# Kernel tuning notes

Measured on AMD Instinct MI355X. Metric: run time of the kernel, lower is better.

Reference implementation:

```python
import jax, jax.numpy as jnp
import numpy as np
from jax import lax

B_, L_, D_ = 4, 2048, 256
DI, NS, DC, DTR = 512, 16, 4, 16  # d_inner=2*D, d_state, d_conv, dt_rank=ceil(D/16)
DFF = 4 * D_


def setup_inputs():
    key = jax.random.key(0)
    ks = jax.random.split(key, 20)
    rn = lambda k, s, sc=0.02: jax.random.normal(k, s, jnp.float32) * sc
    return {
        "x": jax.random.normal(ks[0], (B_, L_, D_), jnp.float32),
        "in_proj_w": rn(ks[1], (2 * DI, D_)), "in_proj_b": jnp.zeros((2 * DI,), jnp.float32),
        "conv_w": rn(ks[2], (DI, DC), 0.1), "conv_b": jnp.zeros((DI,), jnp.float32),
        "x_proj_w": rn(ks[3], (DTR + 2 * NS, DI)),
        "dt_proj_w": rn(ks[4], (DI, DTR), 0.1), "dt_proj_b": rn(ks[5], (DI,), 0.5),
        "A_log": jnp.log(jnp.tile(jnp.arange(1, NS + 1, dtype=jnp.float32), (DI, 1))),
        "D_ssm": jnp.ones((DI,), jnp.float32),
        "out_proj_w": rn(ks[6], (D_, DI)), "out_proj_b": jnp.zeros((D_,), jnp.float32),
        "ln1_g": jnp.ones((D_,), jnp.float32), "ln1_b": jnp.zeros((D_,), jnp.float32),
        "fc1_w": rn(ks[7], (DFF, D_)), "fc1_b": jnp.zeros((DFF,), jnp.float32),
        "fc2_w": rn(ks[8], (D_, DFF)), "fc2_b": jnp.zeros((D_,), jnp.float32),
        "ln2_g": jnp.ones((D_,), jnp.float32), "ln2_b": jnp.zeros((D_,), jnp.float32),
    }


def _layer_norm(x, g, b, eps=1e-5):
    m = jnp.mean(x, -1, keepdims=True)
    v = jnp.mean((x - m) ** 2, -1, keepdims=True)
    return (x - m) / jnp.sqrt(v + eps) * g + b


def _mamba(x, in_proj_w, in_proj_b, conv_w, conv_b, x_proj_w, dt_proj_w, dt_proj_b, A_log, D_ssm, out_proj_w, out_proj_b):
    B, L, D = x.shape
    xz = x @ in_proj_w.T + in_proj_b                       # [B,L,2*DI]
    xi, z = jnp.split(xz, 2, axis=-1)
    # causal depthwise conv over time
    xc = jnp.transpose(xi, (0, 2, 1))                       # [B,DI,L]
    xc = lax.conv_general_dilated(xc, conv_w[:, None, :], (1,), [(DC - 1, 0)],
                                  dimension_numbers=("NCH", "OIH", "NCH"),
                                  feature_group_count=DI)
    xi = jax.nn.silu(jnp.transpose(xc + conv_b[None, :, None], (0, 2, 1)))  # [B,L,DI]
    x_dbl = xi @ x_proj_w.T                                 # [B,L,DTR+2*NS]
    dt, Bs, Cs = jnp.split(x_dbl, [DTR, DTR + NS], axis=-1)
    dt = jax.nn.softplus(dt @ dt_proj_w.T + dt_proj_b)      # [B,L,DI]
    A = -jnp.exp(A_log)                                     # [DI,NS]
    dA = jnp.exp(dt[..., None] * A)                         # [B,L,DI,NS]
    dBu = dt[..., None] * Bs[:, :, None, :] * xi[..., None]  # [B,L,DI,NS]
    dA_t = jnp.moveaxis(dA, 1, 0)
    dBu_t = jnp.moveaxis(dBu, 1, 0)
    C_t = jnp.moveaxis(Cs, 1, 0)                            # [L,B,NS]

    def step(h, inp):
        a, bu, c = inp
        h = a * h + bu                                      # [B,DI,NS]
        y = jnp.einsum("bdn,bn->bd", h, c)
        return h, y

    h0 = jnp.zeros((B, DI, NS), x.dtype)
    _, ys = lax.scan(step, h0, (dA_t, dBu_t, C_t))
    y = jnp.moveaxis(ys, 0, 1) + xi * D_ssm                 # [B,L,DI]
    y = y * jax.nn.silu(z)
    return y @ out_proj_w.T + out_proj_b


def reference(x, in_proj_w, in_proj_b, conv_w, conv_b, x_proj_w, dt_proj_w, dt_proj_b,
              A_log, D_ssm, out_proj_w, out_proj_b, ln1_g, ln1_b, fc1_w, fc1_b,
              fc2_w, fc2_b, ln2_g, ln2_b):
    gelu = lambda t: jax.nn.gelu(t, approximate=False)
    ssm = _mamba(x, in_proj_w, in_proj_b, conv_w, conv_b, x_proj_w, dt_proj_w,
                 dt_proj_b, A_log, D_ssm, out_proj_w, out_proj_b)
    y = _layer_norm(x + ssm, ln1_g, ln1_b)                  # dropout = identity (eval)
    ffn = gelu(gelu(y @ fc1_w.T + fc1_b) @ fc2_w.T + fc2_b)
    return _layer_norm(y + ffn, ln2_g, ln2_b)
```

## Files before the change

### kernel.cpp

```cpp
#include <hip/hip_runtime.h>

typedef __bf16 bf16x8 __attribute__((ext_vector_type(8)));
typedef float  f32x4  __attribute__((ext_vector_type(4)));

#define AS1 __attribute__((address_space(1)))
#define AS3 __attribute__((address_space(3)))

__device__ __forceinline__ float bf2f(ushort u) {
    union { unsigned int i; float f; } v; v.i = ((unsigned int)u) << 16; return v.f;
}
__device__ __forceinline__ ushort f2bf(float f) {
    union { float f; unsigned int i; } v; v.f = f;
    unsigned int i = v.i;
    unsigned int r = i + 0x7FFFu + ((i >> 16) & 1u);
    return (ushort)(r >> 16);
}
__device__ __forceinline__ float bflo(unsigned int u) { return bf2f((ushort)(u & 0xFFFFu)); }
__device__ __forceinline__ float bfhi(unsigned int u) { return bf2f((ushort)(u >> 16)); }

__device__ __forceinline__ bool sniff_inline(const ushort* __restrict__ x) {
    const int lane = threadIdx.x & 63;
    int cnt = 0;
    #pragma unroll
    for (int r = 0; r < 4; r++) {
        const ushort u = x[lane + r * 64];
        const int e = (u >> 7) & 0xFF;
        if ((u & 0x7FFF) == 0 || (e >= 112 && e <= 141)) cnt++;
    }
    #pragma unroll
    for (int o = 32; o > 0; o >>= 1) cnt += __shfl_xor(cnt, o);
    return cnt >= 224;
}

struct CanonArgs {
    const void* src[20];
    int off[20];
    int total;
};

__launch_bounds__(256)
__global__ void canon_k(CanonArgs a, ushort* __restrict__ dst, ushort* __restrict__ xpw_pad,
                        const ushort* __restrict__ sniffx)
{
    const int i = blockIdx.x * 256 + threadIdx.x;
    if (i >= a.total) {
        const int j = i - a.total;
        if (j < 8192) xpw_pad[24576 + j] = 0;
        return;
    }
    const bool fl = sniff_inline(sniffx);
    int s = 0;
    #pragma unroll
    for (int t = 1; t < 20; t++) if (i >= a.off[t]) s = t;
    const int li = i - a.off[s];
    ushort v;
    if (fl) v = ((const ushort*)a.src[s])[li];
    else    v = f2bf(((const float*)a.src[s])[li]);
    dst[i] = v;
    if (s == 5) xpw_pad[li] = v;
}

template<int BM, int BN, int ACT, bool HASB, bool WF32, bool WBF16>
__launch_bounds__(256, 2)
__global__ void gemm_bt(const ushort* __restrict__ A, const ushort* __restrict__ W,
                        const ushort* __restrict__ bias,
                        float* __restrict__ Cf, ushort* __restrict__ Cb,
                        int M, int N, int K, int lda)
{
    constexpr int WMT = BM / 32;
    constexpr int WNT = BN / 32;
    __shared__ __align__(16) ushort As[BM * 32];
    __shared__ __align__(16) ushort Bs[BN * 32];
    const int tid  = threadIdx.x;
    const int wave = tid >> 6;
    const int lane = tid & 63;
    const int m0 = blockIdx.x * BM;
    const int n0 = blockIdx.y * BN;
    const int wm = (wave >> 1) * (BM / 2);
    const int wn = (wave & 1) * (BN / 2);
    const int lrow = lane & 15;
    const int quad = lane >> 4;

    f32x4 acc[WMT][WNT];
    #pragma unroll
    for (int i = 0; i < WMT; i++)
        #pragma unroll
        for (int j = 0; j < WNT; j++)
            #pragma unroll
            for (int r = 0; r < 4; r++) acc[i][j][r] = 0.f;

    for (int k0 = 0; k0 < K; k0 += 32) {
        #pragma unroll
        for (int t = 0; t < BM / 64; t++) {
            const int inst = t * 4 + wave;
            const int row  = inst * 16 + (lane >> 2);
            const int sub  = lane & 3;
            const ushort* gp = A + (size_t)(m0 + row) * lda + (k0 + sub * 8);
            __builtin_amdgcn_global_load_lds((AS1 void*)(void*)gp,
                                             (AS3 void*)(As + inst * 512), 16, 0, 0);
        }
        #pragma unroll
        for (int t = 0; t < BN / 64; t++) {
            const int inst = t * 4 + wave;
            const int row  = inst * 16 + (lane >> 2);
            const int sub  = lane & 3;
            const ushort* gp = W + (size_t)(n0 + row) * K + (k0 + sub * 8);
            __builtin_amdgcn_global_load_lds((AS1 void*)(void*)gp,
                                             (AS3 void*)(Bs + inst * 512), 16, 0, 0);
        }
        __syncthreads();
        bf16x8 afr[WMT], bfr[WNT];
        #pragma unroll
        for (int i = 0; i < WMT; i++)
            afr[i] = *(const bf16x8*)&As[(wm + i * 16 + lrow) * 32 + quad * 8];
        #pragma unroll
        for (int j = 0; j < WNT; j++)
            bfr[j] = *(const bf16x8*)&Bs[(wn + j * 16 + lrow) * 32 + quad * 8];
        #pragma unroll
        for (int i = 0; i < WMT; i++)
            #pragma unroll
            for (int j = 0; j < WNT; j++)
                acc[i][j] = __builtin_amdgcn_mfma_f32_16x16x32_bf16(afr[i], bfr[j], acc[i][j], 0, 0, 0);
        __syncthreads();
    }

    #pragma unroll
    for (int i = 0; i < WMT; i++) {
        const int gm = m0 + wm + i * 16 + quad * 4;
        #pragma unroll
        for (int j = 0; j < WNT; j++) {
            const int gn = n0 + wn + j * 16 + lrow;
            const float bv = HASB ? bf2f(bias[gn]) : 0.f;
            #pragma unroll
            for (int r = 0; r < 4; r++) {
                float v = acc[i][j][r] + bv;
                if (ACT == 1) v = 0.5f * v * (1.f + erff(v * 0.70710678118654752f));
                const size_t off = (size_t)(gm + r) * N + gn;
                if (WF32)  Cf[off] = v;
                if (WBF16) Cb[off] = f2bf(v);
            }
        }
    }
}

__launch_bounds__(256, 2)
__global__ void convxdbl_k(const ushort* __restrict__ xz, const ushort* __restrict__ cw,
                           const ushort* __restrict__ cb, const ushort* __restrict__ xpw_pad,
                           ushort* __restrict__ xc, float* __restrict__ xdbl)
{
    __shared__ __align__(16) ushort xcs[16 * 520];
    __shared__ __align__(16) ushort Bs[64 * 32];
    const int tid  = threadIdx.x;
    const int wave = tid >> 6;
    const int lane = tid & 63;
    const int T0 = blockIdx.x * 16;

    const int d8 = (tid & 63) * 8;
    const int tr = tid >> 6;
    ushort wl[32];
    *(uint4*)&wl[0]  = *(const uint4*)&cw[d8 * 4];
    *(uint4*)&wl[8]  = *(const uint4*)&cw[d8 * 4 + 8];
    *(uint4*)&wl[16] = *(const uint4*)&cw[d8 * 4 + 16];
    *(uint4*)&wl[24] = *(const uint4*)&cw[d8 * 4 + 24];
    ushort bl[8];
    *(uint4*)&bl[0] = *(const uint4*)&cb[d8];
    #pragma unroll
    for (int it = 0; it < 4; it++) {
        const int trow = it * 4 + tr;
        const int t = T0 + trow;
        const int l = t & 2047;
        float acc[8];
        #pragma unroll
        for (int j = 0; j < 8; j++) acc[j] = bf2f(bl[j]);
        #pragma unroll
        for (int k = 0; k < 4; k++) {
            const int ls = l - 3 + k;
            if (ls >= 0) {
                ushort xl[8];
                *(uint4*)&xl[0] = *(const uint4*)&xz[(size_t)(t - 3 + k) * 1024 + d8];
                #pragma unroll
                for (int j = 0; j < 8; j++) acc[j] += bf2f(xl[j]) * bf2f(wl[j * 4 + k]);
            }
        }
        ushort ol[8];
        #pragma unroll
        for (int j = 0; j < 8; j++) {
            const float s = acc[j] / (1.f + __expf(-acc[j]));
            ol[j] = f2bf(s);
        }
        *(uint4*)&xcs[trow * 520 + d8] = *(uint4*)&ol[0];
        *(uint4*)&xc[(size_t)t * 512 + d8] = *(uint4*)&ol[0];
    }
    __syncthreads();

    const int lrow = lane & 15;
    const int quad = lane >> 4;
    const int wn = wave * 16;
    f32x4 acc2 = {0.f, 0.f, 0.f, 0.f};
    for (int k0 = 0; k0 < 512; k0 += 32) {
        {
            const int row = wn + (lane >> 2);
            const int sub = lane & 3;
            const ushort* gp = xpw_pad + (size_t)row * 512 + (k0 + sub * 8);
            __builtin_amdgcn_global_load_lds((AS1 void*)(void*)gp,
                                             (AS3 void*)(Bs + wave * 512), 16, 0, 0);
        }
        __syncthreads();
        const bf16x8 afr = *(const bf16x8*)&xcs[lrow * 520 + k0 + quad * 8];
        const bf16x8 bfr = *(const bf16x8*)&Bs[wave * 512 + lrow * 32 + quad * 8];
        acc2 = __builtin_amdgcn_mfma_f32_16x16x32_bf16(afr, bfr, acc2, 0, 0, 0);
        __syncthreads();
    }
    #pragma unroll
    for (int r = 0; r < 4; r++)
        xdbl[(size_t)(T0 + quad * 4 + r) * 64 + wn + lrow] = acc2[r];
}

__launch_bounds__(256)
__global__ void scan1_k(const float* __restrict__ xdbl, const ushort* __restrict__ xc,
                        const ushort* __restrict__ dtw, const ushort* __restrict__ dtb,
                        const ushort* __restrict__ Alog, float* __restrict__ summ)
{
    __shared__ float XD[32 * 32];
    const int tid = threadIdx.x;
    const int c = blockIdx.y, b = blockIdx.z;
    const int t0 = b * 2048 + c * 32;
    for (int e = tid; e < 1024; e += 256)
        XD[e] = xdbl[(size_t)(t0 + (e >> 5)) * 64 + (e & 31)];
    __syncthreads();
    const int d = blockIdx.x * 256 + tid;

    const uint4 w0 = *(const uint4*)&dtw[d * 16];
    const uint4 w1 = *(const uint4*)&dtw[d * 16 + 8];
    const float wd[16] = { bflo(w0.x), bfhi(w0.x), bflo(w0.y), bfhi(w0.y),
                           bflo(w0.z), bfhi(w0.z), bflo(w0.w), bfhi(w0.w),
                           bflo(w1.x), bfhi(w1.x), bflo(w1.y), bfhi(w1.y),
                           bflo(w1.z), bfhi(w1.z), bflo(w1.w), bfhi(w1.w) };
    const float dtbv = bf2f(dtb[d]);

    float A[16], h[16];
    #pragma unroll
    for (int n = 0; n < 16; n++) {
        A[n] = -__expf(bf2f(Alog[d * 16 + n]));
        h[n] = 0.f;
    }
    float sdt = 0.f;
    for (int i = 0; i < 32; i++) {
        const float* Xr = &XD[i * 32];
        float s = dtbv;
        #pragma unroll
        for (int k = 0; k < 16; k++) s += Xr[k] * wd[k];
        const float dtv = (s > 15.f) ? s : __logf(1.f + __expf(s));
        const float xiv = bf2f(xc[(size_t)(t0 + i) * 512 + d]);
        const float dx = dtv * xiv;
        sdt += dtv;
        #pragma unroll
        for (int n = 0; n < 16; n++) {
            const float da = __expf(dtv * A[n]);
            h[n] = da * h[n] + dx * Xr[16 + n];
        }
    }
    const size_t base = ((size_t)(b * 64 + c) * 32) * 512 + d;
    #pragma unroll
    for (int n = 0; n < 16; n++) summ[base + (size_t)n * 512] = __expf(A[n] * sdt);
    #pragma unroll
    for (int n = 0; n < 16; n++) summ[base + (size_t)(16 + n) * 512] = h[n];
}

__launch_bounds__(512)
__global__ void combine_k(float* __restrict__ summ)
{
    const int b = blockIdx.x >> 4, n = blockIdx.x & 15;
    const int d = threadIdx.x;
    float h = 0.f;
    #pragma unroll
    for (int half = 0; half < 2; half++) {
        float p[32], hl[32], ho[32];
        #pragma unroll
        for (int c2 = 0; c2 < 32; c2++) {
            const size_t sb = ((size_t)((b * 64 + half * 32 + c2) * 32 + n)) * 512 + d;
            p[c2]  = summ[sb];
            hl[c2] = summ[sb + 8192];
        }
        #pragma unroll
        for (int c2 = 0; c2 < 32; c2++) {
            ho[c2] = h;
            h = p[c2] * h + hl[c2];
        }
        #pragma unroll
        for (int c2 = 0; c2 < 32; c2++) {
            const size_t sb = ((size_t)((b * 64 + half * 32 + c2) * 32 + n)) * 512 + d;
            summ[sb] = ho[c2];
        }
    }
}

__launch_bounds__(256)
__global__ void scan2_k(const float* __restrict__ xdbl, ushort* xc,
                        const ushort* __restrict__ dtw, const ushort* __restrict__ dtb,
                        const ushort* __restrict__ Alog, const float* __restrict__ summ,
                        const ushort* __restrict__ xz, const ushort* __restrict__ Dssm)
{
    __shared__ float XD[32 * 48];
    const int tid = threadIdx.x;
    const int c = blockIdx.y, b = blockIdx.z;
    const int t0 = b * 2048 + c * 32;
    for (int e = tid; e < 1536; e += 256)
        XD[e] = xdbl[(size_t)(t0 + (e / 48)) * 64 + (e % 48)];
    __syncthreads();
    const int d = blockIdx.x * 256 + tid;

    const uint4 w0 = *(const uint4*)&dtw[d * 16];
    const uint4 w1 = *(const uint4*)&dtw[d * 16 + 8];
    const float wd[16] = { bflo(w0.x), bfhi(w0.x), bflo(w0.y), bfhi(w0.y),
                           bflo(w0.z), bfhi(w0.z), bflo(w0.w), bfhi(w0.w),
                           bflo(w1.x), bfhi(w1.x), bflo(w1.y), bfhi(w1.y),
                           bflo(w1.z), bfhi(w1.z), bflo(w1.w), bfhi(w1.w) };
    const float dtbv = bf2f(dtb[d]);

    float A[16], h[16];
    #pragma unroll
    for (int n = 0; n < 16; n++) A[n] = -__expf(bf2f(Alog[d * 16 + n]));
    const size_t base = ((size_t)(b * 64 + c) * 32) * 512 + d;
    #pragma unroll
    for (int n = 0; n < 16; n++) h[n] = summ[base + (size_t)n * 512];
    const float Dv = bf2f(Dssm[d]);

    for (int i = 0; i < 32; i++) {
        const int t = t0 + i;
        const float* Xr = &XD[i * 48];
        float s = dtbv;
        #pragma unroll
        for (int k = 0; k < 16; k++) s += Xr[k] * wd[k];
        const float dtv = (s > 15.f) ? s : __logf(1.f + __expf(s));
        const float xiv = bf2f(xc[(size_t)t * 512 + d]);
        const float dx = dtv * xiv;
        float yv = 0.f;
        #pragma unroll
        for (int n = 0; n < 16; n++) {
            const float da = __expf(dtv * A[n]);
            h[n] = da * h[n] + dx * Xr[16 + n];
            yv += h[n] * Xr[32 + n];
        }
        yv += xiv * Dv;
        const float zv = bf2f(xz[(size_t)t * 1024 + 512 + d]);
        yv *= zv / (1.f + __expf(-zv));
        xc[(size_t)t * 512 + d] = f2bf(yv);
    }
}

template<int K, int ACT, int MODE>
__launch_bounds__(256, 2)
__global__ void gemm_ln16(const ushort* __restrict__ A, const ushort* __restrict__ W,
                          const ushort* __restrict__ bias,
                          const ushort* __restrict__ residb, const float* __restrict__ residf,
                          const ushort* __restrict__ g, const ushort* __restrict__ bvec,
                          float* __restrict__ y1f_out, ushort* __restrict__ y1b_out,
                          void* __restrict__ dout, const ushort* __restrict__ sniffx)
{
    __shared__ __align__(16) ushort As[16 * 32];
    __shared__ __align__(16) ushort Bs[256 * 32];
    __shared__ float redS[64], redQ[64];
    const int tid  = threadIdx.x;
    const int wave = tid >> 6;
    const int lane = tid & 63;
    const int lrow = lane & 15;
    const int quad = lane >> 4;
    const int m0 = blockIdx.x * 16;
    const int wn = wave * 64;

    f32x4 acc[4];
    #pragma unroll
    for (int j = 0; j < 4; j++)
        #pragma unroll
        for (int r = 0; r < 4; r++) acc[j][r] = 0.f;

    for (int k0 = 0; k0 < K; k0 += 32) {
        if (wave == 0) {
            const int row = lane >> 2;
            const int sub = lane & 3;
            const ushort* gp = A + (size_t)(m0 + row) * K + (k0 + sub * 8);
            __builtin_amdgcn_global_load_lds((AS1 void*)(void*)gp,
                                             (AS3 void*)(As), 16, 0, 0);
        }
        #pragma unroll
        for (int t = 0; t < 4; t++) {
            const int inst = t * 4 + wave;
            const int row  = inst * 16 + (lane >> 2);
            const int sub  = lane & 3;
            const ushort* gp = W + (size_t)row * K + (k0 + sub * 8);
            __builtin_amdgcn_global_load_lds((AS1 void*)(void*)gp,
                                             (AS3 void*)(Bs + inst * 512), 16, 0, 0);
        }
        __syncthreads();
        const bf16x8 afr = *(const bf16x8*)&As[lrow * 32 + quad * 8];
        #pragma unroll
        for (int j = 0; j < 4; j++) {
            const bf16x8 bfr = *(const bf16x8*)&Bs[(wn + j * 16 + lrow) * 32 + quad * 8];
            acc[j] = __builtin_amdgcn_mfma_f32_16x16x32_bf16(afr, bfr, acc[j], 0, 0, 0);
        }
        __syncthreads();
    }

    float v[4][4];
    float ps[4] = {0.f, 0.f, 0.f, 0.f}, pq[4] = {0.f, 0.f, 0.f, 0.f};
    #pragma unroll
    for (int j = 0; j < 4; j++) {
        const int gn = wn + j * 16 + lrow;
        const float bv = bf2f(bias[gn]);
        #pragma unroll
        for (int r = 0; r < 4; r++) {
            const size_t off = (size_t)(m0 + quad * 4 + r) * 256 + gn;
            float x_ = acc[j][r] + bv;
            if (ACT == 1) x_ = 0.5f * x_ * (1.f + erff(x_ * 0.70710678118654752f));
            x_ += (MODE == 0) ? bf2f(residb[off]) : residf[off];
            v[j][r] = x_;
            ps[r] += x_;
            pq[r] += x_ * x_;
        }
    }
    #pragma unroll
    for (int r = 0; r < 4; r++) {
        #pragma unroll
        for (int o = 8; o > 0; o >>= 1) {
            ps[r] += __shfl_xor(ps[r], o);
            pq[r] += __shfl_xor(pq[r], o);
        }
    }
    if (lrow == 0) {
        #pragma unroll
        for (int r = 0; r < 4; r++) {
            redS[wave * 16 + quad * 4 + r] = ps[r];
            redQ[wave * 16 + quad * 4 + r] = pq[r];
        }
    }
    __syncthreads();

    const bool fl = (MODE == 1) ? sniff_inline(sniffx) : false;
    #pragma unroll
    for (int r = 0; r < 4; r++) {
        const int row = quad * 4 + r;
        const float S = redS[row] + redS[16 + row] + redS[32 + row] + redS[48 + row];
        const float Q = redQ[row] + redQ[16 + row] + redQ[32 + row] + redQ[48 + row];
        const float mean = S * (1.f / 256.f);
        const float var  = Q * (1.f / 256.f) - mean * mean;
        const float rs   = rsqrtf(var + 1e-5f);
        #pragma unroll
        for (int j = 0; j < 4; j++) {
            const int gn = wn + j * 16 + lrow;
            const size_t off = (size_t)(m0 + row) * 256 + gn;
            const float out = (v[j][r] - mean) * rs * bf2f(g[gn]) + bf2f(bvec[gn]);
            if (MODE == 0) {
                y1f_out[off] = out;
                y1b_out[off] = f2bf(out);
            } else {
                if (fl) ((ushort*)dout)[off] = f2bf(out);
                else    ((float*)dout)[off]  = out;
            }
        }
    }
}

extern "C" void kernel_launch(void* const* d_in, const int* in_sizes, int n_in,
                              void* d_out, int out_size, void* d_ws, size_t ws_size,
                              hipStream_t stream)
{
    char* ws = (char*)d_ws;
    ushort* canon = (ushort*)(ws + 256);

    static const int coff[20] = {
        0,        2097152,  2359296,  2360320,  2362368,
        2362880,  2387456,  2395648,  2396160,  2404352,
        2404864,  2535936,  2536192,  2536448,  2536704,
        2798848,  2799872,  3062016,  3062272,  3062528 };
    static const int ctot = 3062784;

    CanonArgs ca;
    for (int i = 0; i < 20; i++) { ca.src[i] = d_in[i]; ca.off[i] = coff[i]; }
    ca.total = ctot;

    const ushort* cx   = canon + coff[0];
    const ushort* cipw = canon + coff[1];
    const ushort* cipb = canon + coff[2];
    const ushort* ccw  = canon + coff[3];
    const ushort* ccb  = canon + coff[4];
    const ushort* cdtw = canon + coff[6];
    const ushort* cdtb = canon + coff[7];
    const ushort* calog= canon + coff[8];
    const ushort* cdssm= canon + coff[9];
    const ushort* copw = canon + coff[10];
    const ushort* copb = canon + coff[11];
    const ushort* cln1g= canon + coff[12];
    const ushort* cln1b= canon + coff[13];
    const ushort* cf1w = canon + coff[14];
    const ushort* cf1b = canon + coff[15];
    const ushort* cf2w = canon + coff[16];
    const ushort* cf2b = canon + coff[17];
    const ushort* cln2g= canon + coff[18];
    const ushort* cln2b= canon + coff[19];

    ushort* xpw_pad = (ushort*)(ws + 6291456);
    ushort* xz      = (ushort*)(ws + 8388608);
    ushort* xc      = (ushort*)(ws + 25165824);
    float*  xdbl    = (float*)(ws + 33554432);
    float*  summ    = (float*)(ws + 35651584);
    float*  y1f     = (float*)(ws + 52428800);
    ushort* y1b     = (ushort*)(ws + 60817408);
    ushort* f1      = (ushort*)(ws + 65011712);
    ushort* yb      = xc;
    const ushort* sx = (const ushort*)d_in[0];

    canon_k<<<(ctot + 8192 + 255) / 256, 256, 0, stream>>>(ca, canon, xpw_pad, sx);
    gemm_bt<128, 128, 0, true, false, true><<<dim3(64, 8), 256, 0, stream>>>(
        cx, cipw, cipb, nullptr, xz, 8192, 1024, 256, 256);
    convxdbl_k<<<512, 256, 0, stream>>>(xz, ccw, ccb, xpw_pad, xc, xdbl);
    scan1_k<<<dim3(2, 64, 4), 256, 0, stream>>>(xdbl, xc, cdtw, cdtb, calog, summ);
    combine_k<<<64, 512, 0, stream>>>(summ);
    scan2_k<<<dim3(2, 64, 4), 256, 0, stream>>>(xdbl, xc, cdtw, cdtb, calog, summ, xz, cdssm);
    gemm_ln16<512, 0, 0><<<512, 256, 0, stream>>>(
        yb, copw, copb, cx, nullptr, cln1g, cln1b, y1f, y1b, nullptr, sx);
    gemm_bt<128, 128, 1, true, false, true><<<dim3(64, 8), 256, 0, stream>>>(
        y1b, cf1w, cf1b, nullptr, f1, 8192, 1024, 256, 256);
    gemm_ln16<1024, 1, 1><<<512, 256, 0, stream>>>(
        f1, cf2w, cf2b, nullptr, y1f, cln2g, cln2b, nullptr, nullptr, d_out, sx);
}
```

Before: 251.7 us.

## Fuse conv, x_proj and chunk scan; fuse scan2 with out_proj, LN and FFN tail

Merges the causal conv, x_proj GEMM and first-pass chunk scan into one kernel per 32-token chunk, so the conv output stays in LDS instead of going to global memory. Merges the second scan pass with out_proj, LN1, fc1+GELU, fc2+GELU and LN2 into a single tail kernel. The FFN intermediate is processed in 256-wide slices held in LDS, which removes the f1, y1 and xc global round-trips and cuts the launch count from 9 to 5. In exchange only 256 blocks run, and weights are read straight from global into MFMA operands rather than staged through LDS, so occupancy and weight bandwidth may limit it. The conv is also recomputed in the tail kernel.

```diff
diff --git a/kernel.cpp b/kernel.cpp
--- a/kernel.cpp
+++ b/kernel.cpp
@@ -17,6 +17,9 @@
 }
 __device__ __forceinline__ float bflo(unsigned int u) { return bf2f((ushort)(u & 0xFFFFu)); }
 __device__ __forceinline__ float bfhi(unsigned int u) { return bf2f((ushort)(u >> 16)); }
+__device__ __forceinline__ float gelu_f(float v) {
+    return 0.5f * v * (1.f + erff(v * 0.70710678118654752f));
+}
 
 __device__ __forceinline__ bool sniff_inline(const ushort* __restrict__ x) {
     const int lane = threadIdx.x & 63;
@@ -60,12 +63,11 @@
     if (s == 5) xpw_pad[li] = v;
 }
 
-template<int BM, int BN, int ACT, bool HASB, bool WF32, bool WBF16>
+template<int BM, int BN>
 __launch_bounds__(256, 2)
 __global__ void gemm_bt(const ushort* __restrict__ A, const ushort* __restrict__ W,
-                        const ushort* __restrict__ bias,
-                        float* __restrict__ Cf, ushort* __restrict__ Cb,
-                        int M, int N, int K, int lda)
+                        const ushort* __restrict__ bias, ushort* __restrict__ Cb,
+                        int N, int K)
 {
     constexpr int WMT = BM / 32;
     constexpr int WNT = BN / 32;
@@ -95,7 +97,7 @@
             const int inst = t * 4 + wave;
             const int row  = inst * 16 + (lane >> 2);
             const int sub  = lane & 3;
-            const ushort* gp = A + (size_t)(m0 + row) * lda + (k0 + sub * 8);
+            const ushort* gp = A + (size_t)(m0 + row) * K + (k0 + sub * 8);
             __builtin_amdgcn_global_load_lds((AS1 void*)(void*)gp,
                                              (AS3 void*)(As + inst * 512), 16, 0, 0);
         }
@@ -130,141 +132,126 @@
         #pragma unroll
         for (int j = 0; j < WNT; j++) {
             const int gn = n0 + wn + j * 16 + lrow;
-            const float bv = HASB ? bf2f(bias[gn]) : 0.f;
-            #pragma unroll
-            for (int r = 0; r < 4; r++) {
-                float v = acc[i][j][r] + bv;
-                if (ACT == 1) v = 0.5f * v * (1.f + erff(v * 0.70710678118654752f));
-                const size_t off = (size_t)(gm + r) * N + gn;
-                if (WF32)  Cf[off] = v;
-                if (WBF16) Cb[off] = f2bf(v);
-            }
-        }
-    }
-}
-
-__launch_bounds__(256, 2)
-__global__ void convxdbl_k(const ushort* __restrict__ xz, const ushort* __restrict__ cw,
-                           const ushort* __restrict__ cb, const ushort* __restrict__ xpw_pad,
-                           ushort* __restrict__ xc, float* __restrict__ xdbl)
+            const float bv = bf2f(bias[gn]);
+            #pragma unroll
+            for (int r = 0; r < 4; r++)
+                Cb[(size_t)(gm + r) * N + gn] = f2bf(acc[i][j][r] + bv);
+        }
+    }
+}
+
+__launch_bounds__(512)
+__global__ void convscan1_k(const ushort* __restrict__ xz, const ushort* __restrict__ cw,
+                            const ushort* __restrict__ cb, const ushort* __restrict__ xpw_pad,
+                            const ushort* __restrict__ dtw, const ushort* __restrict__ dtb,
+                            const ushort* __restrict__ Alog,
+                            float* __restrict__ xdbl, float* __restrict__ summ)
 {
-    __shared__ __align__(16) ushort xcs[16 * 520];
-    __shared__ __align__(16) ushort Bs[64 * 32];
+    __shared__ __align__(16) ushort xcs[32 * 520];
+    __shared__ float XD[32 * 48];
     const int tid  = threadIdx.x;
     const int wave = tid >> 6;
     const int lane = tid & 63;
-    const int T0 = blockIdx.x * 16;
-
-    const int d8 = (tid & 63) * 8;
-    const int tr = tid >> 6;
-    ushort wl[32];
-    *(uint4*)&wl[0]  = *(const uint4*)&cw[d8 * 4];
-    *(uint4*)&wl[8]  = *(const uint4*)&cw[d8 * 4 + 8];
-    *(uint4*)&wl[16] = *(const uint4*)&cw[d8 * 4 + 16];
-    *(uint4*)&wl[24] = *(const uint4*)&cw[d8 * 4 + 24];
-    ushort bl[8];
-    *(uint4*)&bl[0] = *(const uint4*)&cb[d8];
-    #pragma unroll
-    for (int it = 0; it < 4; it++) {
-        const int trow = it * 4 + tr;
-        const int t = T0 + trow;
-        const int l = t & 2047;
-        float acc[8];
-        #pragma unroll
-        for (int j = 0; j < 8; j++) acc[j] = bf2f(bl[j]);
-        #pragma unroll
-        for (int k = 0; k < 4; k++) {
-            const int ls = l - 3 + k;
-            if (ls >= 0) {
-                ushort xl[8];
-                *(uint4*)&xl[0] = *(const uint4*)&xz[(size_t)(t - 3 + k) * 1024 + d8];
-                #pragma unroll
-                for (int j = 0; j < 8; j++) acc[j] += bf2f(xl[j]) * bf2f(wl[j * 4 + k]);
-            }
-        }
-        ushort ol[8];
-        #pragma unroll
-        for (int j = 0; j < 8; j++) {
-            const float s = acc[j] / (1.f + __expf(-acc[j]));
-            ol[j] = f2bf(s);
-        }
-        *(uint4*)&xcs[trow * 520 + d8] = *(uint4*)&ol[0];
-        *(uint4*)&xc[(size_t)t * 512 + d8] = *(uint4*)&ol[0];
-    }
-    __syncthreads();
-
     const int lrow = lane & 15;
     const int quad = lane >> 4;
-    const int wn = wave * 16;
-    f32x4 acc2 = {0.f, 0.f, 0.f, 0.f};
-    for (int k0 = 0; k0 < 512; k0 += 32) {
-        {
-            const int row = wn + (lane >> 2);
-            const int sub = lane & 3;
-            const ushort* gp = xpw_pad + (size_t)row * 512 + (k0 + sub * 8);
-            __builtin_amdgcn_global_load_lds((AS1 void*)(void*)gp,
-                                             (AS3 void*)(Bs + wave * 512), 16, 0, 0);
-        }
-        __syncthreads();
-        const bf16x8 afr = *(const bf16x8*)&xcs[lrow * 520 + k0 + quad * 8];
-        const bf16x8 bfr = *(const bf16x8*)&Bs[wave * 512 + lrow * 32 + quad * 8];
-        acc2 = __builtin_amdgcn_mfma_f32_16x16x32_bf16(afr, bfr, acc2, 0, 0, 0);
-        __syncthreads();
-    }
-    #pragma unroll
-    for (int r = 0; r < 4; r++)
-        xdbl[(size_t)(T0 + quad * 4 + r) * 64 + wn + lrow] = acc2[r];
-}
-
-__launch_bounds__(256)
-__global__ void scan1_k(const float* __restrict__ xdbl, const ushort* __restrict__ xc,
-                        const ushort* __restrict__ dtw, const ushort* __restrict__ dtb,
-                        const ushort* __restrict__ Alog, float* __restrict__ summ)
-{
-    __shared__ float XD[32 * 32];
-    const int tid = threadIdx.x;
-    const int c = blockIdx.y, b = blockIdx.z;
+    const int c = blockIdx.x, b = blockIdx.y;
     const int t0 = b * 2048 + c * 32;
-    for (int e = tid; e < 1024; e += 256)
-        XD[e] = xdbl[(size_t)(t0 + (e >> 5)) * 64 + (e & 31)];
+
+    {
+        const int d8 = (tid & 63) * 8;
+        ushort wl[32];
+        *(uint4*)&wl[0]  = *(const uint4*)&cw[d8 * 4];
+        *(uint4*)&wl[8]  = *(const uint4*)&cw[d8 * 4 + 8];
+        *(uint4*)&wl[16] = *(const uint4*)&cw[d8 * 4 + 16];
+        *(uint4*)&wl[24] = *(const uint4*)&cw[d8 * 4 + 24];
+        ushort bl[8];
+        *(uint4*)&bl[0] = *(const uint4*)&cb[d8];
+        #pragma unroll
+        for (int it = 0; it < 4; it++) {
+            const int trow = it * 8 + (tid >> 6);
+            const int t = t0 + trow;
+            const int l = t & 2047;
+            float acc[8];
+            #pragma unroll
+            for (int j = 0; j < 8; j++) acc[j] = bf2f(bl[j]);
+            #pragma unroll
+            for (int k = 0; k < 4; k++) {
+                const int ls = l - 3 + k;
+                if (ls >= 0) {
+                    ushort xl[8];
+                    *(uint4*)&xl[0] = *(const uint4*)&xz[(size_t)(t - 3 + k) * 1024 + d8];
+                    #pragma unroll
+                    for (int j = 0; j < 8; j++) acc[j] += bf2f(xl[j]) * bf2f(wl[j * 4 + k]);
+                }
+            }
+            ushort ol[8];
+            #pragma unroll
+            for (int j = 0; j < 8; j++) {
+                const float s = acc[j] / (1.f + __expf(-acc[j]));
+                ol[j] = f2bf(s);
+            }
+            *(uint4*)&xcs[trow * 520 + d8] = *(uint4*)&ol[0];
+        }
+    }
     __syncthreads();
-    const int d = blockIdx.x * 256 + tid;
-
-    const uint4 w0 = *(const uint4*)&dtw[d * 16];
-    const uint4 w1 = *(const uint4*)&dtw[d * 16 + 8];
-    const float wd[16] = { bflo(w0.x), bfhi(w0.x), bflo(w0.y), bfhi(w0.y),
-                           bflo(w0.z), bfhi(w0.z), bflo(w0.w), bfhi(w0.w),
-                           bflo(w1.x), bfhi(w1.x), bflo(w1.y), bfhi(w1.y),
-                           bflo(w1.z), bfhi(w1.z), bflo(w1.w), bfhi(w1.w) };
-    const float dtbv = bf2f(dtb[d]);
-
-    float A[16], h[16];
-    #pragma unroll
-    for (int n = 0; n < 16; n++) {
-        A[n] = -__expf(bf2f(Alog[d * 16 + n]));
-        h[n] = 0.f;
-    }
-    float sdt = 0.f;
-    for (int i = 0; i < 32; i++) {
-        const float* Xr = &XD[i * 32];
-        float s = dtbv;
-        #pragma unroll
-        for (int k = 0; k < 16; k++) s += Xr[k] * wd[k];
-        const float dtv = (s > 15.f) ? s : __logf(1.f + __expf(s));
-        const float xiv = bf2f(xc[(size_t)(t0 + i) * 512 + d]);
-        const float dx = dtv * xiv;
-        sdt += dtv;
+
+    {
+        const int mt = wave >> 2, nt = wave & 3;
+        f32x4 acc = {0.f, 0.f, 0.f, 0.f};
+        for (int k0 = 0; k0 < 512; k0 += 32) {
+            const bf16x8 afr = *(const bf16x8*)&xcs[(mt * 16 + lrow) * 520 + k0 + quad * 8];
+            const bf16x8 bfr = *(const bf16x8*)(xpw_pad + (size_t)(nt * 16 + lrow) * 512 + k0 + quad * 8);
+            acc = __builtin_amdgcn_mfma_f32_16x16x32_bf16(afr, bfr, acc, 0, 0, 0);
+        }
+        const int col = nt * 16 + lrow;
+        if (col < 48) {
+            #pragma unroll
+            for (int r = 0; r < 4; r++) {
+                const int row = mt * 16 + quad * 4 + r;
+                XD[row * 48 + col] = acc[r];
+                xdbl[(size_t)(t0 + row) * 64 + col] = acc[r];
+            }
+        }
+    }
+    __syncthreads();
+
+    {
+        const int d = tid;
+        const uint4 w0 = *(const uint4*)&dtw[d * 16];
+        const uint4 w1 = *(const uint4*)&dtw[d * 16 + 8];
+        const float wd[16] = { bflo(w0.x), bfhi(w0.x), bflo(w0.y), bfhi(w0.y),
+                               bflo(w0.z), bfhi(w0.z), bflo(w0.w), bfhi(w0.w),
+                               bflo(w1.x), bfhi(w1.x), bflo(w1.y), bfhi(w1.y),
+                               bflo(w1.z), bfhi(w1.z), bflo(w1.w), bfhi(w1.w) };
+        const float dtbv = bf2f(dtb[d]);
+        float A[16], h[16];
         #pragma unroll
         for (int n = 0; n < 16; n++) {
-            const float da = __expf(dtv * A[n]);
-            h[n] = da * h[n] + dx * Xr[16 + n];
-        }
-    }
-    const size_t base = ((size_t)(b * 64 + c) * 32) * 512 + d;
-    #pragma unroll
-    for (int n = 0; n < 16; n++) summ[base + (size_t)n * 512] = __expf(A[n] * sdt);
-    #pragma unroll
-    for (int n = 0; n < 16; n++) summ[base + (size_t)(16 + n) * 512] = h[n];
+            A[n] = -__expf(bf2f(Alog[d * 16 + n]));
+            h[n] = 0.f;
+        }
+        float sdt = 0.f;
+        for (int i = 0; i < 32; i++) {
+            const float* Xr = &XD[i * 48];
+            float s = dtbv;
+            #pragma unroll
+            for (int k = 0; k < 16; k++) s += Xr[k] * wd[k];
+            const float dtv = (s > 15.f) ? s : __logf(1.f + __expf(s));
+            const float xiv = bf2f(xcs[i * 520 + d]);
+            const float dx = dtv * xiv;
+            sdt += dtv;
+            #pragma unroll
+            for (int n = 0; n < 16; n++) {
+                const float da = __expf(dtv * A[n]);
+                h[n] = da * h[n] + dx * Xr[16 + n];
+            }
+        }
+        const size_t base = ((size_t)(b * 64 + c) * 32) * 512 + d;
+        #pragma unroll
+        for (int n = 0; n < 16; n++) summ[base + (size_t)n * 512] = __expf(A[n] * sdt);
+        #pragma unroll
+        for (int n = 0; n < 16; n++) summ[base + (size_t)(16 + n) * 512] = h[n];
+    }
 }
 
 __launch_bounds__(512)
@@ -295,167 +282,312 @@
     }
 }
 
-__launch_bounds__(256)
-__global__ void scan2_k(const float* __restrict__ xdbl, ushort* xc,
-                        const ushort* __restrict__ dtw, const ushort* __restrict__ dtb,
-                        const ushort* __restrict__ Alog, const float* __restrict__ summ,
-                        const ushort* __restrict__ xz, const ushort* __restrict__ Dssm)
+__launch_bounds__(512)
+__global__ void tail_k(const ushort* __restrict__ xz, const ushort* __restrict__ cw,
+                       const ushort* __restrict__ cb, const float* __restrict__ xdbl,
+                       const ushort* __restrict__ dtw, const ushort* __restrict__ dtb,
+                       const ushort* __restrict__ Alog, const float* __restrict__ summ,
+                       const ushort* __restrict__ Dssm, const ushort* __restrict__ cx,
+                       const ushort* __restrict__ opw, const ushort* __restrict__ opb,
+                       const ushort* __restrict__ ln1g, const ushort* __restrict__ ln1b,
+                       const ushort* __restrict__ f1w, const ushort* __restrict__ f1b,
+                       const ushort* __restrict__ f2w, const ushort* __restrict__ f2b,
+                       const ushort* __restrict__ ln2g, const ushort* __restrict__ ln2b,
+                       void* __restrict__ dout, const ushort* __restrict__ sniffx)
 {
+    __shared__ __align__(16) ushort yls[32 * 520];
     __shared__ float XD[32 * 48];
-    const int tid = threadIdx.x;
-    const int c = blockIdx.y, b = blockIdx.z;
-    const int t0 = b * 2048 + c * 32;
-    for (int e = tid; e < 1536; e += 256)
-        XD[e] = xdbl[(size_t)(t0 + (e / 48)) * 64 + (e % 48)];
-    __syncthreads();
-    const int d = blockIdx.x * 256 + tid;
-
-    const uint4 w0 = *(const uint4*)&dtw[d * 16];
-    const uint4 w1 = *(const uint4*)&dtw[d * 16 + 8];
-    const float wd[16] = { bflo(w0.x), bfhi(w0.x), bflo(w0.y), bfhi(w0.y),
-                           bflo(w0.z), bfhi(w0.z), bflo(w0.w), bfhi(w0.w),
-                           bflo(w1.x), bfhi(w1.x), bflo(w1.y), bfhi(w1.y),
-                           bflo(w1.z), bfhi(w1.z), bflo(w1.w), bfhi(w1.w) };
-    const float dtbv = bf2f(dtb[d]);
-
-    float A[16], h[16];
-    #pragma unroll
-    for (int n = 0; n < 16; n++) A[n] = -__expf(bf2f(Alog[d * 16 + n]));
-    const size_t base = ((size_t)(b * 64 + c) * 32) * 512 + d;
-    #pragma unroll
-    for (int n = 0; n < 16; n++) h[n] = summ[base + (size_t)n * 512];
-    const float Dv = bf2f(Dssm[d]);
-
-    for (int i = 0; i < 32; i++) {
-        const int t = t0 + i;
-        const float* Xr = &XD[i * 48];
-        float s = dtbv;
-        #pragma unroll
-        for (int k = 0; k < 16; k++) s += Xr[k] * wd[k];
-        const float dtv = (s > 15.f) ? s : __logf(1.f + __expf(s));
-        const float xiv = bf2f(xc[(size_t)t * 512 + d]);
-        const float dx = dtv * xiv;
-        float yv = 0.f;
-        #pragma unroll
-        for (int n = 0; n < 16; n++) {
-            const float da = __expf(dtv * A[n]);
-            h[n] = da * h[n] + dx * Xr[16 + n];
-            yv += h[n] * Xr[32 + n];
-        }
-        yv += xiv * Dv;
-        const float zv = bf2f(xz[(size_t)t * 1024 + 512 + d]);
-        yv *= zv / (1.f + __expf(-zv));
-        xc[(size_t)t * 512 + d] = f2bf(yv);
-    }
-}
-
-template<int K, int ACT, int MODE>
-__launch_bounds__(256, 2)
-__global__ void gemm_ln16(const ushort* __restrict__ A, const ushort* __restrict__ W,
-                          const ushort* __restrict__ bias,
-                          const ushort* __restrict__ residb, const float* __restrict__ residf,
-                          const ushort* __restrict__ g, const ushort* __restrict__ bvec,
-                          float* __restrict__ y1f_out, ushort* __restrict__ y1b_out,
-                          void* __restrict__ dout, const ushort* __restrict__ sniffx)
-{
-    __shared__ __align__(16) ushort As[16 * 32];
-    __shared__ __align__(16) ushort Bs[256 * 32];
-    __shared__ float redS[64], redQ[64];
+    __shared__ __align__(16) ushort y1bs[32 * 264];
+    __shared__ float redS[8 * 32], redQ[8 * 32];
+    ushort* f1q = yls;
+
     const int tid  = threadIdx.x;
     const int wave = tid >> 6;
     const int lane = tid & 63;
     const int lrow = lane & 15;
     const int quad = lane >> 4;
-    const int m0 = blockIdx.x * 16;
-    const int wn = wave * 64;
-
-    f32x4 acc[4];
-    #pragma unroll
-    for (int j = 0; j < 4; j++)
-        #pragma unroll
-        for (int r = 0; r < 4; r++) acc[j][r] = 0.f;
-
-    for (int k0 = 0; k0 < K; k0 += 32) {
-        if (wave == 0) {
-            const int row = lane >> 2;
-            const int sub = lane & 3;
-            const ushort* gp = A + (size_t)(m0 + row) * K + (k0 + sub * 8);
-            __builtin_amdgcn_global_load_lds((AS1 void*)(void*)gp,
-                                             (AS3 void*)(As), 16, 0, 0);
-        }
-        #pragma unroll
-        for (int t = 0; t < 4; t++) {
-            const int inst = t * 4 + wave;
-            const int row  = inst * 16 + (lane >> 2);
-            const int sub  = lane & 3;
-            const ushort* gp = W + (size_t)row * K + (k0 + sub * 8);
-            __builtin_amdgcn_global_load_lds((AS1 void*)(void*)gp,
-                                             (AS3 void*)(Bs + inst * 512), 16, 0, 0);
-        }
+    const int c = blockIdx.x, b = blockIdx.y;
+    const int t0 = b * 2048 + c * 32;
+
+    {
+        const int d8 = (tid & 63) * 8;
+        ushort wl[32];
+        *(uint4*)&wl[0]  = *(const uint4*)&cw[d8 * 4];
+        *(uint4*)&wl[8]  = *(const uint4*)&cw[d8 * 4 + 8];
+        *(uint4*)&wl[16] = *(const uint4*)&cw[d8 * 4 + 16];
+        *(uint4*)&wl[24] = *(const uint4*)&cw[d8 * 4 + 24];
+        ushort bl[8];
+        *(uint4*)&bl[0] = *(const uint4*)&cb[d8];
+        #pragma unroll
+        for (int it = 0; it < 4; it++) {
+            const int trow = it * 8 + (tid >> 6);
+            const int t = t0 + trow;
+            const int l = t & 2047;
+            float acc[8];
+            #pragma unroll
+            for (int j = 0; j < 8; j++) acc[j] = bf2f(bl[j]);
+            #pragma unroll
+            for (int k = 0; k < 4; k++) {
+                const int ls = l - 3 + k;
+                if (ls >= 0) {
+                    ushort xl[8];
+                    *(uint4*)&xl[0] = *(const uint4*)&xz[(size_t)(t - 3 + k) * 1024 + d8];
+                    #pragma unroll
+                    for (int j = 0; j < 8; j++) acc[j] += bf2f(xl[j]) * bf2f(wl[j * 4 + k]);
+                }
+            }
+            ushort ol[8];
+            #pragma unroll
+            for (int j = 0; j < 8; j++) {
+                const float s = acc[j] / (1.f + __expf(-acc[j]));
+                ol[j] = f2bf(s);
+            }
+            *(uint4*)&yls[trow * 520 + d8] = *(uint4*)&ol[0];
+        }
+    }
+    for (int e = tid; e < 1536; e += 512)
+        XD[e] = xdbl[(size_t)(t0 + (e / 48)) * 64 + (e % 48)];
+    __syncthreads();
+
+    {
+        const int d = tid;
+        const uint4 w0 = *(const uint4*)&dtw[d * 16];
+        const uint4 w1 = *(const uint4*)&dtw[d * 16 + 8];
+        const float wd[16] = { bflo(w0.x), bfhi(w0.x), bflo(w0.y), bfhi(w0.y),
+                               bflo(w0.z), bfhi(w0.z), bflo(w0.w), bfhi(w0.w),
+                               bflo(w1.x), bfhi(w1.x), bflo(w1.y), bfhi(w1.y),
+                               bflo(w1.z), bfhi(w1.z), bflo(w1.w), bfhi(w1.w) };
+        const float dtbv = bf2f(dtb[d]);
+        float A[16], h[16];
+        #pragma unroll
+        for (int n = 0; n < 16; n++) A[n] = -__expf(bf2f(Alog[d * 16 + n]));
+        const size_t base = ((size_t)(b * 64 + c) * 32) * 512 + d;
+        #pragma unroll
+        for (int n = 0; n < 16; n++) h[n] = summ[base + (size_t)n * 512];
+        const float Dv = bf2f(Dssm[d]);
+        for (int i = 0; i < 32; i++) {
+            const int t = t0 + i;
+            const float* Xr = &XD[i * 48];
+            float s = dtbv;
+            #pragma unroll
+            for (int k = 0; k < 16; k++) s += Xr[k] * wd[k];
+            const float dtv = (s > 15.f) ? s : __logf(1.f + __expf(s));
+            const float xiv = bf2f(yls[i * 520 + d]);
+            const float dx = dtv * xiv;
+            float yv = 0.f;
+            #pragma unroll
+            for (int n = 0; n < 16; n++) {
+                const float da = __expf(dtv * A[n]);
+                h[n] = da * h[n] + dx * Xr[16 + n];
+                yv += h[n] * Xr[32 + n];
+            }
+            yv += xiv * Dv;
+            const float zv = bf2f(xz[(size_t)t * 1024 + 512 + d]);
+            yv *= zv / (1.f + __expf(-zv));
+            yls[i * 520 + d] = f2bf(yv);
+        }
+    }
+    __syncthreads();
+
+    const int n0w = wave * 32;
+    f32x4 accP[2][2];
+    #pragma unroll
+    for (int i = 0; i < 2; i++)
+        #pragma unroll
+        for (int j = 0; j < 2; j++)
+            #pragma unroll
+            for (int r = 0; r < 4; r++) accP[i][j][r] = 0.f;
+    for (int k0 = 0; k0 < 512; k0 += 32) {
+        bf16x8 afr[2], bfr[2];
+        #pragma unroll
+        for (int i = 0; i < 2; i++)
+            afr[i] = *(const bf16x8*)&yls[(i * 16 + lrow) * 520 + k0 + quad * 8];
+        #pragma unroll
+        for (int j = 0; j < 2; j++)
+            bfr[j] = *(const bf16x8*)(opw + (size_t)(n0w + j * 16 + lrow) * 512 + k0 + quad * 8);
+        #pragma unroll
+        for (int i = 0; i < 2; i++)
+            #pragma unroll
+            for (int j = 0; j < 2; j++)
+                accP[i][j] = __builtin_amdgcn_mfma_f32_16x16x32_bf16(afr[i], bfr[j], accP[i][j], 0, 0, 0);
+    }
+    float vP[2][2][4];
+    float ps[2][4], pq[2][4];
+    #pragma unroll
+    for (int i = 0; i < 2; i++)
+        #pragma unroll
+        for (int r = 0; r < 4; r++) { ps[i][r] = 0.f; pq[i][r] = 0.f; }
+    #pragma unroll
+    for (int i = 0; i < 2; i++) {
+        #pragma unroll
+        for (int j = 0; j < 2; j++) {
+            const int col = n0w + j * 16 + lrow;
+            const float bv = bf2f(opb[col]);
+            #pragma unroll
+            for (int r = 0; r < 4; r++) {
+                const int row = i * 16 + quad * 4 + r;
+                float v = accP[i][j][r] + bv + bf2f(cx[(size_t)(t0 + row) * 256 + col]);
+                vP[i][j][r] = v;
+                ps[i][r] += v;
+                pq[i][r] += v * v;
+            }
+        }
+    }
+    #pragma unroll
+    for (int i = 0; i < 2; i++)
+        #pragma unroll
+        for (int r = 0; r < 4; r++) {
+            #pragma unroll
+            for (int o = 8; o > 0; o >>= 1) {
+                ps[i][r] += __shfl_xor(ps[i][r], o);
+                pq[i][r] += __shfl_xor(pq[i][r], o);
+            }
+            if (lrow == 0) {
+                const int row = i * 16 + quad * 4 + r;
+                redS[wave * 32 + row] = ps[i][r];
+                redQ[wave * 32 + row] = pq[i][r];
+            }
+        }
+    __syncthreads();
+
+    float y1f[2][2][4];
+    #pragma unroll
+    for (int i = 0; i < 2; i++) {
+        #pragma unroll
+        for (int r = 0; r < 4; r++) {
+            const int row = i * 16 + quad * 4 + r;
+            float S = 0.f, Q = 0.f;
+            #pragma unroll
+            for (int w = 0; w < 8; w++) { S += redS[w * 32 + row]; Q += redQ[w * 32 + row]; }
+            const float mean = S * (1.f / 256.f);
+            const float var  = Q * (1.f / 256.f) - mean * mean;
+            const float rs   = rsqrtf(var + 1e-5f);
+            #pragma unroll
+            for (int j = 0; j < 2; j++) {
+                const int col = n0w + j * 16 + lrow;
+                const float o2 = (vP[i][j][r] - mean) * rs * bf2f(ln1g[col]) + bf2f(ln1b[col]);
+                y1f[i][j][r] = o2;
+                y1bs[row * 264 + col] = f2bf(o2);
+            }
+        }
+    }
+    __syncthreads();
+
+    f32x4 acc2[2][2];
+    #pragma unroll
+    for (int i = 0; i < 2; i++)
+        #pragma unroll
+        for (int j = 0; j < 2; j++)
+            #pragma unroll
+            for (int r = 0; r < 4; r++) acc2[i][j][r] = 0.f;
+
+    for (int q = 0; q < 4; q++) {
+        f32x4 a1[2][2];
+        #pragma unroll
+        for (int i = 0; i < 2; i++)
+            #pragma unroll
+            for (int j = 0; j < 2; j++)
+                #pragma unroll
+                for (int r = 0; r < 4; r++) a1[i][j][r] = 0.f;
+        for (int k0 = 0; k0 < 256; k0 += 32) {
+            bf16x8 afr[2], bfr[2];
+            #pragma unroll
+            for (int i = 0; i < 2; i++)
+                afr[i] = *(const bf16x8*)&y1bs[(i * 16 + lrow) * 264 + k0 + quad * 8];
+            #pragma unroll
+            for (int j = 0; j < 2; j++)
+                bfr[j] = *(const bf16x8*)(f1w + (size_t)(q * 256 + n0w + j * 16 + lrow) * 256 + k0 + quad * 8);
+            #pragma unroll
+            for (int i = 0; i < 2; i++)
+                #pragma unroll
+                for (int j = 0; j < 2; j++)
+                    a1[i][j] = __builtin_amdgcn_mfma_f32_16x16x32_bf16(afr[i], bfr[j], a1[i][j], 0, 0, 0);
+        }
+        #pragma unroll
+        for (int i = 0; i < 2; i++)
+            #pragma unroll
+            for (int j = 0; j < 2; j++) {
+                const int qc = n0w + j * 16 + lrow;
+                const float bv = bf2f(f1b[q * 256 + qc]);
+                #pragma unroll
+                for (int r = 0; r < 4; r++) {
+                    const int row = i * 16 + quad * 4 + r;
+                    f1q[row * 260 + qc] = f2bf(gelu_f(a1[i][j][r] + bv));
+                }
+            }
         __syncthreads();
-        const bf16x8 afr = *(const bf16x8*)&As[lrow * 32 + quad * 8];
-        #pragma unroll
-        for (int j = 0; j < 4; j++) {
-            const bf16x8 bfr = *(const bf16x8*)&Bs[(wn + j * 16 + lrow) * 32 + quad * 8];
-            acc[j] = __builtin_amdgcn_mfma_f32_16x16x32_bf16(afr, bfr, acc[j], 0, 0, 0);
+        for (int k0 = 0; k0 < 256; k0 += 32) {
+            bf16x8 afr[2], bfr[2];
+            #pragma unroll
+            for (int i = 0; i < 2; i++)
+                afr[i] = *(const bf16x8*)&f1q[(i * 16 + lrow) * 260 + k0 + quad * 8];
+            #pragma unroll
+            for (int j = 0; j < 2; j++)
+                bfr[j] = *(const bf16x8*)(f2w + (size_t)(n0w + j * 16 + lrow) * 1024 + q * 256 + k0 + quad * 8);
+            #pragma unroll
+            for (int i = 0; i < 2; i++)
+                #pragma unroll
+                for (int j = 0; j < 2; j++)
+                    acc2[i][j] = __builtin_amdgcn_mfma_f32_16x16x32_bf16(afr[i], bfr[j], acc2[i][j], 0, 0, 0);
         }
         __syncthreads();
     }
 
-    float v[4][4];
-    float ps[4] = {0.f, 0.f, 0.f, 0.f}, pq[4] = {0.f, 0.f, 0.f, 0.f};
-    #pragma unroll
-    for (int j = 0; j < 4; j++) {
-        const int gn = wn + j * 16 + lrow;
-        const float bv = bf2f(bias[gn]);
+    float v2[2][2][4];
+    #pragma unroll
+    for (int i = 0; i < 2; i++)
+        #pragma unroll
+        for (int r = 0; r < 4; r++) { ps[i][r] = 0.f; pq[i][r] = 0.f; }
+    #pragma unroll
+    for (int i = 0; i < 2; i++)
+        #pragma unroll
+        for (int j = 0; j < 2; j++) {
+            const int col = n0w + j * 16 + lrow;
+            const float bv = bf2f(f2b[col]);
+            #pragma unroll
+            for (int r = 0; r < 4; r++) {
+                const float v = gelu_f(acc2[i][j][r] + bv) + y1f[i][j][r];
+                v2[i][j][r] = v;
+                ps[i][r] += v;
+                pq[i][r] += v * v;
+            }
+        }
+    #pragma unroll
+    for (int i = 0; i < 2; i++)
         #pragma unroll
         for (int r = 0; r < 4; r++) {
-            const size_t off = (size_t)(m0 + quad * 4 + r) * 256 + gn;
-            float x_ = acc[j][r] + bv;
-            if (ACT == 1) x_ = 0.5f * x_ * (1.f + erff(x_ * 0.70710678118654752f));
-            x_ += (MODE == 0) ? bf2f(residb[off]) : residf[off];
-            v[j][r] = x_;
-            ps[r] += x_;
-            pq[r] += x_ * x_;
-        }
-    }
-    #pragma unroll
-    for (int r = 0; r < 4; r++) {
-        #pragma unroll
-        for (int o = 8; o > 0; o >>= 1) {
-            ps[r] += __shfl_xor(ps[r], o);
-            pq[r] += __shfl_xor(pq[r], o);
-        }
-    }
-    if (lrow == 0) {
+            #pragma unroll
+            for (int o = 8; o > 0; o >>= 1) {
+                ps[i][r] += __shfl_xor(ps[i][r], o);
+                pq[i][r] += __shfl_xor(pq[i][r], o);
+            }
+            if (lrow == 0) {
+                const int row = i * 16 + quad * 4 + r;
+                redS[wave * 32 + row] = ps[i][r];
+                redQ[wave * 32 + row] = pq[i][r];
+            }
+        }
+    __syncthreads();
+
+    const bool fl = sniff_inline(sniffx);
+    #pragma unroll
+    for (int i = 0; i < 2; i++) {
         #pragma unroll
         for (int r = 0; r < 4; r++) {
-            redS[wave * 16 + quad * 4 + r] = ps[r];
-            redQ[wave * 16 + quad * 4 + r] = pq[r];
-        }
-    }
-    __syncthreads();
-
-    const bool fl = (MODE == 1) ? sniff_inline(sniffx) : false;
-    #pragma unroll
-    for (int r = 0; r < 4; r++) {
-        const int row = quad * 4 + r;
-        const float S = redS[row] + redS[16 + row] + redS[32 + row] + redS[48 + row];
-        const float Q = redQ[row] + redQ[16 + row] + redQ[32 + row] + redQ[48 + row];
-        const float mean = S * (1.f / 256.f);
-        const float var  = Q * (1.f / 256.f) - mean * mean;
-        const float rs   = rsqrtf(var + 1e-5f);
-        #pragma unroll
-        for (int j = 0; j < 4; j++) {
-            const int gn = wn + j * 16 + lrow;
-            const size_t off = (size_t)(m0 + row) * 256 + gn;
-            const float out = (v[j][r] - mean) * rs * bf2f(g[gn]) + bf2f(bvec[gn]);
-            if (MODE == 0) {
-                y1f_out[off] = out;
-                y1b_out[off] = f2bf(out);
-            } else {
-                if (fl) ((ushort*)dout)[off] = f2bf(out);
-                else    ((float*)dout)[off]  = out;
+            const int row = i * 16 + quad * 4 + r;
+            float S = 0.f, Q = 0.f;
+            #pragma unroll
+            for (int w = 0; w < 8; w++) { S += redS[w * 32 + row]; Q += redQ[w * 32 + row]; }
+            const float mean = S * (1.f / 256.f);
+            const float var  = Q * (1.f / 256.f) - mean * mean;
+            const float rs   = rsqrtf(var + 1e-5f);
+            #pragma unroll
+            for (int j = 0; j < 2; j++) {
+                const int col = n0w + j * 16 + lrow;
+                const size_t off = (size_t)(t0 + row) * 256 + col;
+                const float o2 = (v2[i][j][r] - mean) * rs * bf2f(ln2g[col]) + bf2f(ln2b[col]);
+                if (fl) ((ushort*)dout)[off] = f2bf(o2);
+                else    ((float*)dout)[off]  = o2;
             }
         }
     }
@@ -501,26 +633,17 @@
 
     ushort* xpw_pad = (ushort*)(ws + 6291456);
     ushort* xz      = (ushort*)(ws + 8388608);
-    ushort* xc      = (ushort*)(ws + 25165824);
-    float*  xdbl    = (float*)(ws + 33554432);
-    float*  summ    = (float*)(ws + 35651584);
-    float*  y1f     = (float*)(ws + 52428800);
-    ushort* y1b     = (ushort*)(ws + 60817408);
-    ushort* f1      = (ushort*)(ws + 65011712);
-    ushort* yb      = xc;
+    float*  xdbl    = (float*)(ws + 25165824);
+    float*  summ    = (float*)(ws + 27262976);
     const ushort* sx = (const ushort*)d_in[0];
 
     canon_k<<<(ctot + 8192 + 255) / 256, 256, 0, stream>>>(ca, canon, xpw_pad, sx);
-    gemm_bt<128, 128, 0, true, false, true><<<dim3(64, 8), 256, 0, stream>>>(
-        cx, cipw, cipb, nullptr, xz, 8192, 1024, 256, 256);
-    convxdbl_k<<<512, 256, 0, stream>>>(xz, ccw, ccb, xpw_pad, xc, xdbl);
-    scan1_k<<<dim3(2, 64, 4), 256, 0, stream>>>(xdbl, xc, cdtw, cdtb, calog, summ);
+    gemm_bt<128, 128><<<dim3(64, 8), 256, 0, stream>>>(cx, cipw, cipb, xz, 1024, 256);
+    convscan1_k<<<dim3(64, 4), 512, 0, stream>>>(
+        xz, ccw, ccb, xpw_pad, cdtw, cdtb, calog, xdbl, summ);
     combine_k<<<64, 512, 0, stream>>>(summ);
-    scan2_k<<<dim3(2, 64, 4), 256, 0, stream>>>(xdbl, xc, cdtw, cdtb, calog, summ, xz, cdssm);
-    gemm_ln16<512, 0, 0><<<512, 256, 0, stream>>>(
-        yb, copw, copb, cx, nullptr, cln1g, cln1b, y1f, y1b, nullptr, sx);
-    gemm_bt<128, 128, 1, true, false, true><<<dim3(64, 8), 256, 0, stream>>>(
-        y1b, cf1w, cf1b, nullptr, f1, 8192, 1024, 256, 256);
-    gemm_ln16<1024, 1, 1><<<512, 256, 0, stream>>>(
-        f1, cf2w, cf2b, nullptr, y1f, cln2g, cln2b, nullptr, nullptr, d_out, sx);
-}
+    tail_k<<<dim3(64, 4), 512, 0, stream>>>(
+        xz, ccw, ccb, xdbl, cdtw, cdtb, calog, summ, cdssm, cx,
+        copw, copb, cln1g, cln1b, cf1w, cf1b, cf2w, cf2b, cln2g, cln2b,
+        d_out, sx);
+}
```

Measured after the change: 237.4 us. 1.06x faster.
